# Kernel tuning notes

Measured on AMD Instinct MI355X. Metric: run time of the kernel, lower is better.

The kernel has to match this reference:

```python
import jax, jax.numpy as jnp
import numpy as np

VOCAB = 4096
CODE_DIM = 3


def setup_inputs() -> dict:
    key = jax.random.key(0)
    k1, k2 = jax.random.split(key)
    B, L = 4, 16384
    feats = jax.random.normal(k1, (B, L, CODE_DIM), dtype=jnp.float32)
    # xavier_uniform init for the (vocab, code_dim) embedding table
    limit = float(np.sqrt(6.0 / (VOCAB + CODE_DIM)))
    codebook = jax.random.uniform(k2, (VOCAB, CODE_DIM), dtype=jnp.float32,
                                  minval=-limit, maxval=limit)
    return {"feats": feats, "codebook": codebook}


def reference(feats, codebook):
    """EMAVQ.forward (eval mode): cdist -> argmin -> gather -> vq loss -> straight-through."""
    B, L, D = feats.shape
    flat = feats.reshape(-1, D)                      # (N, D)
    dist = (jnp.sum(flat * flat, axis=1, keepdims=True)
            - 2.0 * (flat @ codebook.T)
            + jnp.sum(codebook * codebook, axis=1))  # (N, V)
    idx = jnp.argmin(dist, axis=1)                   # (N,)
    quant = codebook[idx].reshape(B, L, D)           # embedding gather
    sg = jax.lax.stop_gradient
    loss = (jnp.mean((quant - sg(feats)) ** 2)
            + 0.25 * jnp.mean((feats - sg(quant)) ** 2))
    quant_st = feats + sg(quant - feats)             # straight-through estimator
    return quant_st, idx.reshape(B, L), loss
```

## Files before the change

### kernel.cpp

```cpp
#include <hip/hip_runtime.h>

#define VOCAB 4096
#define SLICES 16
#define SLICE 256
#define TRK 32
#define NSUP (SLICE / TRK)
#define P 2
#define PTS (64 * P)
#define THREADS 1024

typedef float f2 __attribute__((ext_vector_type(2)));

__device__ __forceinline__ f2 fma2(f2 a, f2 b, f2 c) {
  return __builtin_elementwise_fma(a, b, c);
}
__device__ __forceinline__ f2 max2(f2 a, f2 b) {
  return __builtin_elementwise_max(a, b);
}

__device__ __forceinline__ float opaque(float x) {
  asm volatile("" : "+v"(x));
  return x;
}

__device__ __forceinline__ float med3f(float a, float b, float c) {
  float d;
  asm("v_med3_f32 %0, %1, %2, %3" : "=v"(d) : "v"(a), "v"(b), "v"(c));
  return d;
}

struct CPair { f2 e0, e1, e2, h; };

__global__ __launch_bounds__(256) void vq_prep_kernel(
    const float* __restrict__ cb, float4* __restrict__ cw,
    float* __restrict__ cwp, float* __restrict__ loss_slot) {
  int j = blockIdx.x * 256 + threadIdx.x;
  if (j == 0) *loss_slot = 0.0f;
  if (j < VOCAB) {
    float e0 = cb[3 * j + 0];
    float e1 = cb[3 * j + 1];
    float e2 = cb[3 * j + 2];
    float p0 = opaque(e0 * e0);
    float p1 = opaque(e1 * e1);
    float p2 = opaque(e2 * e2);
    float c = opaque(opaque(p0 + p1) + p2);
    float h = -0.5f * c;
    cw[j] = make_float4(e0, e1, e2, h);
    int i = j >> 1, o = j & 1;
    cwp[i * 8 + 0 + o] = e0;
    cwp[i * 8 + 2 + o] = e1;
    cwp[i * 8 + 4 + o] = e2;
    cwp[i * 8 + 6 + o] = h;
  }
}

__device__ __forceinline__ float dist_f32(float x0, float x1, float x2,
                                          float a, float4 cd) {
  float m = fmaf(x2, cd.z, fmaf(x1, cd.y, x0 * cd.x));
  return fmaf(-2.0f, m, a) + (-2.0f * cd.w);
}

__global__ __launch_bounds__(THREADS, 8) void vq_kernel(
    const float* __restrict__ feats, const float4* __restrict__ cw,
    const CPair* __restrict__ cp, float* __restrict__ out_quant,
    float* __restrict__ out_idx, float* __restrict__ out_loss, int npts) {
  __shared__ float sT1[SLICES * PTS];
  __shared__ float sT2[SLICES * PTS];
  __shared__ int sG[SLICES * PTS];
  __shared__ unsigned long long sSlot[PTS];
  __shared__ float4 sFP[PTS];
  __shared__ int sList[PTS];
  __shared__ int sCount;
  __shared__ double sPart[2];

  const int tid = threadIdx.x;
  const int lane = tid & 63;
  const int s = __builtin_amdgcn_readfirstlane(tid >> 6);

  if (tid == 0) sCount = 0;

  const int pbase = blockIdx.x * PTS;
  float px[P], py[P], pz[P], nn[P];
#pragma unroll
  for (int k = 0; k < P; ++k) {
    const int p = pbase + k * 64 + lane;
    px[k] = feats[3 * p + 0];
    py[k] = feats[3 * p + 1];
    pz[k] = feats[3 * p + 2];
    float q0 = opaque(px[k] * px[k]);
    float q1 = opaque(py[k] * py[k]);
    float q2 = opaque(pz[k] * pz[k]);
    nn[k] = opaque(opaque(q0 + q1) + q2);
  }

  f2 X[P], Y[P], Z[P];
#pragma unroll
  for (int k = 0; k < P; ++k) {
    X[k] = (f2){px[k], px[k]};
    Y[k] = (f2){py[k], py[k]};
    Z[k] = (f2){pz[k], pz[k]};
  }
  const CPair* cs = cp + s * (SLICE / 2);
  float t1[P], t2[P];
  int gg[P];
#pragma unroll
  for (int k = 0; k < P; ++k) { t1[k] = -3.4e38f; t2[k] = -3.4e38f; gg[k] = 0; }
#pragma unroll 2
  for (int g = 0; g < NSUP; ++g) {
    const CPair* gp = cs + g * (TRK / 2);
    f2 mm[P];
#pragma unroll
    for (int k = 0; k < P; ++k) mm[k] = (f2){-3.4e38f, -3.4e38f};
#pragma unroll
    for (int c = 0; c < TRK / 8; ++c) {
      const CPair* ck = gp + c * 4;
      CPair a0 = ck[0], a1 = ck[1], a2 = ck[2], a3 = ck[3];
#pragma unroll
      for (int k = 0; k < P; ++k) {
        f2 u0 = fma2(X[k], a0.e0, fma2(Y[k], a0.e1, fma2(Z[k], a0.e2, a0.h)));
        f2 u1 = fma2(X[k], a1.e0, fma2(Y[k], a1.e1, fma2(Z[k], a1.e2, a1.h)));
        f2 u2 = fma2(X[k], a2.e0, fma2(Y[k], a2.e1, fma2(Z[k], a2.e2, a2.h)));
        f2 u3 = fma2(X[k], a3.e0, fma2(Y[k], a3.e1, fma2(Z[k], a3.e2, a3.h)));
        mm[k] = max2(mm[k], max2(max2(u0, u1), max2(u2, u3)));
      }
    }
#pragma unroll
    for (int k = 0; k < P; ++k) {
      float gm = fmaxf(mm[k].x, mm[k].y);
      t2[k] = med3f(t1[k], t2[k], gm);
      if (gm > t1[k]) gg[k] = g;
      t1[k] = fmaxf(t1[k], gm);
    }
  }
#pragma unroll
  for (int k = 0; k < P; ++k) {
    sT1[s * PTS + k * 64 + lane] = t1[k];
    sT2[s * PTS + k * 64 + lane] = t2[k];
    sG[s * PTS + k * 64 + lane] = s * SLICE + gg[k] * TRK;
  }
  __syncthreads();

  int bi = 0;
  float q0 = 0.0f, q1 = 0.0f, q2 = 0.0f;
  bool flagged = false;
  float x0 = px[0], x1 = py[0], x2 = pz[0], a = nn[0];
#pragma unroll
  for (int k = 1; k < P; ++k) {
    if (s == k) { x0 = px[k]; x1 = py[k]; x2 = pz[k]; a = nn[k]; }
  }
  if (tid < PTS) {
    float b1 = sT1[tid], b2 = sT2[tid];
    int gbase = sG[tid];
#pragma unroll
    for (int k = 1; k < SLICES; ++k) {
      float u1 = sT1[k * PTS + tid];
      float u2 = sT2[k * PTS + tid];
      b2 = fmaxf(fmaxf(b2, u2), fminf(b1, u1));
      if (u1 > b1) gbase = sG[k * PTS + tid];
      b1 = fmaxf(b1, u1);
    }
    float eps = fmaf(a, 0x1p-21f, 0x1p-20f);
    flagged = !((b1 - b2) > eps);
    if (flagged) {
      int pos = atomicAdd(&sCount, 1);
      sList[pos] = tid;
      sSlot[tid] = ~0ULL;
      sFP[tid] = make_float4(x0, x1, x2, a);
    } else {
      float bd = 3.4e38f;
#pragma unroll 8
      for (int k = 0; k < TRK; ++k) {
        float4 cd = cw[gbase + k];
        float d = dist_f32(x0, x1, x2, a, cd);
        if (d < bd) { bd = d; bi = gbase + k; q0 = cd.x; q1 = cd.y; q2 = cd.z; }
      }
    }
  }
  __syncthreads();

  const int cnt = sCount;
  for (int f = 0; f < cnt; ++f) {
    const int fpt = sList[f];
    float4 fp = sFP[fpt];
    float y0 = fp.x, y1 = fp.y, y2 = fp.z;
    float ay = fp.w;
    float bd = 3.4e38f;
    int bj = 0;
#pragma unroll
    for (int k = 0; k < VOCAB / THREADS; ++k) {
      int j = tid + k * THREADS;
      float4 cd = cw[j];
      float d = dist_f32(y0, y1, y2, ay, cd);
      if (d < bd) { bd = d; bj = j; }
    }
    unsigned b = __float_as_uint(bd);
    b = (b & 0x80000000u) ? ~b : (b | 0x80000000u);
    unsigned long long key = ((unsigned long long)b << 32) | (unsigned)bj;
#pragma unroll
    for (int off = 1; off < 64; off <<= 1) {
      unsigned long long o = __shfl_xor(key, off);
      key = (o < key) ? o : key;
    }
    if (lane == 0) atomicMin(&sSlot[fpt], key);
  }
  __syncthreads();

  double lsum = 0.0;
  if (tid < PTS) {
    if (flagged) {
      bi = (int)(unsigned)(sSlot[tid] & 0xFFFFFFFFu);
      float4 cd = cw[bi];
      q0 = cd.x; q1 = cd.y; q2 = cd.z;
    }
    const int p = pbase + tid;
    float t0 = q0 - x0, t1d = q1 - x1, t2d = q2 - x2;
    out_quant[3 * p + 0] = x0 + t0;
    out_quant[3 * p + 1] = x1 + t1d;
    out_quant[3 * p + 2] = x2 + t2d;
    out_idx[p] = (float)bi;
    lsum = (double)t0 * t0 + (double)t1d * t1d + (double)t2d * t2d;
  }
#pragma unroll
  for (int off = 32; off >= 1; off >>= 1) lsum += __shfl_down(lsum, off);
  if (lane == 0 && s < P) sPart[s] = lsum;
  __syncthreads();

  if (tid == 0) {
    double acc = sPart[0] + sPart[1];
    atomicAdd(out_loss, (float)(acc * (1.25 / ((double)npts * 3.0))));
  }
}

extern "C" void kernel_launch(void* const* d_in, const int* in_sizes, int n_in,
                              void* d_out, int out_size, void* d_ws,
                              size_t ws_size, hipStream_t stream) {
  const float* feats = (const float*)d_in[0];
  const float* cb = (const float*)d_in[1];
  const int npts = in_sizes[0] / 3;

  float* out = (float*)d_out;
  float* out_quant = out;
  float* out_idx = out + in_sizes[0];
  float* out_loss = out + in_sizes[0] + npts;

  float4* cw = (float4*)d_ws;
  float* cwp = (float*)(cw + VOCAB);

  vq_prep_kernel<<<VOCAB / 256, 256, 0, stream>>>(cb, cw, cwp, out_loss);
  vq_kernel<<<npts / PTS, THREADS, 0, stream>>>(feats, cw, (const CPair*)cwp,
                                                out_quant, out_idx, out_loss,
                                                npts);
}
```

Baseline: 87.75 us.

## Split codebook into e/h chunk arrays and software-pipeline chunk loads

Changes the packed codebook layout into separate per-chunk arrays, one for the three coordinates and one for the half-norm terms. The coarse scan is flattened into a single chunk loop that prefetches the next chunk while the current one is computed, and folds in the per-group top-2 update every four chunks. The goal is to hide global/scalar load latency in the hot distance loop. The prefetch reads one chunk past each slice, which is why a padding chunk (NCHT=513) is reserved, and the extra in-flight registers could raise register pressure.

```diff
diff --git a/kernel.cpp b/kernel.cpp
--- a/kernel.cpp
+++ b/kernel.cpp
@@ -4,10 +4,11 @@
 #define SLICES 16
 #define SLICE 256
 #define TRK 32
-#define NSUP (SLICE / TRK)
+#define NCHUNK 32
 #define P 2
 #define PTS (64 * P)
 #define THREADS 1024
+#define NCHT 513
 
 typedef float f2 __attribute__((ext_vector_type(2)));
 
@@ -29,11 +30,12 @@
   return d;
 }
 
-struct CPair { f2 e0, e1, e2, h; };
+struct EChunk { f2 e0[4], e1[4], e2[4]; };
 
 __global__ __launch_bounds__(256) void vq_prep_kernel(
     const float* __restrict__ cb, float4* __restrict__ cw,
-    float* __restrict__ cwp, float* __restrict__ loss_slot) {
+    float* __restrict__ cwe, float* __restrict__ cwh,
+    float* __restrict__ loss_slot) {
   int j = blockIdx.x * 256 + threadIdx.x;
   if (j == 0) *loss_slot = 0.0f;
   if (j < VOCAB) {
@@ -47,10 +49,11 @@
     float h = -0.5f * c;
     cw[j] = make_float4(e0, e1, e2, h);
     int i = j >> 1, o = j & 1;
-    cwp[i * 8 + 0 + o] = e0;
-    cwp[i * 8 + 2 + o] = e1;
-    cwp[i * 8 + 4 + o] = e2;
-    cwp[i * 8 + 6 + o] = h;
+    int ch = i >> 2, q = i & 3;
+    cwe[ch * 24 + 0 * 8 + q * 2 + o] = e0;
+    cwe[ch * 24 + 1 * 8 + q * 2 + o] = e1;
+    cwe[ch * 24 + 2 * 8 + q * 2 + o] = e2;
+    cwh[ch * 8 + q * 2 + o] = h;
   }
 }
 
@@ -62,8 +65,9 @@
 
 __global__ __launch_bounds__(THREADS, 8) void vq_kernel(
     const float* __restrict__ feats, const float4* __restrict__ cw,
-    const CPair* __restrict__ cp, float* __restrict__ out_quant,
-    float* __restrict__ out_idx, float* __restrict__ out_loss, int npts) {
+    const EChunk* __restrict__ ech, const float4* __restrict__ hch,
+    float* __restrict__ out_quant, float* __restrict__ out_idx,
+    float* __restrict__ out_loss, int npts) {
   __shared__ float sT1[SLICES * PTS];
   __shared__ float sT2[SLICES * PTS];
   __shared__ int sG[SLICES * PTS];
@@ -100,37 +104,48 @@
     Y[k] = (f2){py[k], py[k]};
     Z[k] = (f2){pz[k], pz[k]};
   }
-  const CPair* cs = cp + s * (SLICE / 2);
+  const EChunk* we = ech + s * NCHUNK;
+  unsigned long long wha = (unsigned long long)(hch + s * (NCHUNK * 2));
+  asm volatile("" : "+v"(wha));
+  const float4* wh = (const float4*)wha;
+
   float t1[P], t2[P];
   int gg[P];
-#pragma unroll
-  for (int k = 0; k < P; ++k) { t1[k] = -3.4e38f; t2[k] = -3.4e38f; gg[k] = 0; }
-#pragma unroll 2
-  for (int g = 0; g < NSUP; ++g) {
-    const CPair* gp = cs + g * (TRK / 2);
-    f2 mm[P];
-#pragma unroll
-    for (int k = 0; k < P; ++k) mm[k] = (f2){-3.4e38f, -3.4e38f};
-#pragma unroll
-    for (int c = 0; c < TRK / 8; ++c) {
-      const CPair* ck = gp + c * 4;
-      CPair a0 = ck[0], a1 = ck[1], a2 = ck[2], a3 = ck[3];
+  f2 mm[P];
+#pragma unroll
+  for (int k = 0; k < P; ++k) {
+    t1[k] = -3.4e38f; t2[k] = -3.4e38f; gg[k] = 0;
+    mm[k] = (f2){-3.4e38f, -3.4e38f};
+  }
+
+  EChunk ec = we[0];
+  float4 ha = wh[0], hb = wh[1];
+#pragma unroll 4
+  for (int c = 0; c < NCHUNK; ++c) {
+    EChunk en = we[c + 1];
+    float4 na = wh[2 * c + 2], nb = wh[2 * c + 3];
+    f2 H0 = (f2){ha.x, ha.y}, H1 = (f2){ha.z, ha.w};
+    f2 H2 = (f2){hb.x, hb.y}, H3 = (f2){hb.z, hb.w};
+#pragma unroll
+    for (int k = 0; k < P; ++k) {
+      f2 u0 = fma2(X[k], ec.e0[0], fma2(Y[k], ec.e1[0], fma2(Z[k], ec.e2[0], H0)));
+      f2 u1 = fma2(X[k], ec.e0[1], fma2(Y[k], ec.e1[1], fma2(Z[k], ec.e2[1], H1)));
+      f2 u2 = fma2(X[k], ec.e0[2], fma2(Y[k], ec.e1[2], fma2(Z[k], ec.e2[2], H2)));
+      f2 u3 = fma2(X[k], ec.e0[3], fma2(Y[k], ec.e1[3], fma2(Z[k], ec.e2[3], H3)));
+      f2 tm = max2(max2(u0, u1), max2(u2, u3));
+      mm[k] = ((c & 3) == 0) ? tm : max2(mm[k], tm);
+    }
+    if ((c & 3) == 3) {
+      const int g = c >> 2;
 #pragma unroll
       for (int k = 0; k < P; ++k) {
-        f2 u0 = fma2(X[k], a0.e0, fma2(Y[k], a0.e1, fma2(Z[k], a0.e2, a0.h)));
-        f2 u1 = fma2(X[k], a1.e0, fma2(Y[k], a1.e1, fma2(Z[k], a1.e2, a1.h)));
-        f2 u2 = fma2(X[k], a2.e0, fma2(Y[k], a2.e1, fma2(Z[k], a2.e2, a2.h)));
-        f2 u3 = fma2(X[k], a3.e0, fma2(Y[k], a3.e1, fma2(Z[k], a3.e2, a3.h)));
-        mm[k] = max2(mm[k], max2(max2(u0, u1), max2(u2, u3)));
+        float gm = fmaxf(mm[k].x, mm[k].y);
+        t2[k] = med3f(t1[k], t2[k], gm);
+        if (gm > t1[k]) gg[k] = g;
+        t1[k] = fmaxf(t1[k], gm);
       }
     }
-#pragma unroll
-    for (int k = 0; k < P; ++k) {
-      float gm = fmaxf(mm[k].x, mm[k].y);
-      t2[k] = med3f(t1[k], t2[k], gm);
-      if (gm > t1[k]) gg[k] = g;
-      t1[k] = fmaxf(t1[k], gm);
-    }
+    ec = en; ha = na; hb = nb;
   }
 #pragma unroll
   for (int k = 0; k < P; ++k) {
@@ -244,10 +259,11 @@
   float* out_loss = out + in_sizes[0] + npts;
 
   float4* cw = (float4*)d_ws;
-  float* cwp = (float*)(cw + VOCAB);
-
-  vq_prep_kernel<<<VOCAB / 256, 256, 0, stream>>>(cb, cw, cwp, out_loss);
-  vq_kernel<<<npts / PTS, THREADS, 0, stream>>>(feats, cw, (const CPair*)cwp,
-                                                out_quant, out_idx, out_loss,
-                                                npts);
-}
+  float* cwe = (float*)(cw + VOCAB);
+  float* cwh = cwe + NCHT * 24;
+
+  vq_prep_kernel<<<VOCAB / 256, 256, 0, stream>>>(cb, cw, cwe, cwh, out_loss);
+  vq_kernel<<<npts / PTS, THREADS, 0, stream>>>(
+      feats, cw, (const EChunk*)cwe, (const float4*)cwh, out_quant, out_idx,
+      out_loss, npts);
+}
```

Measured after the change: 94.33 us. +7.5%, slower.
